# Kernel optimization log

Measured on AMD Instinct MI355X. Metric: run time of the kernel, lower is better.

The kernel has to match this reference:

```python
import jax, jax.numpy as jnp
import numpy as np

N_ELEC = 4096
D_IN = 512
D_MODEL = 512
N_HEADS = 8


def setup_inputs() -> dict:
    key = jax.random.key(0)
    ks = jax.random.split(key, 6)
    scale_in = 1.0 / np.sqrt(D_IN)
    scale_model = 1.0 / np.sqrt(D_MODEL)
    return {
        "hs": jax.random.normal(ks[0], (N_ELEC, D_IN), jnp.float32),
        "hd": jax.random.normal(ks[1], (N_ELEC, D_IN), jnp.float32),
        "qk_kernel": jax.random.normal(ks[2], (D_IN, 2 * D_MODEL), jnp.float32) * scale_in,
        "qk_bias": jnp.zeros((2 * D_MODEL,), jnp.float32),
        "v_kernel": jax.random.normal(ks[3], (D_IN, D_MODEL), jnp.float32) * scale_in,
        "v_bias": jnp.zeros((D_MODEL,), jnp.float32),
        "o_kernel": jax.random.normal(ks[4], (D_MODEL, D_MODEL), jnp.float32) * scale_model,
        "o_bias": jnpp if False else jnp.zeros((D_MODEL,), jnp.float32),
    }


def reference(hs, hd, qk_kernel, qk_bias, v_kernel, v_bias, o_kernel, o_bias):
    n_elec = hs.shape[0]
    # projections
    qk = hs @ qk_kernel + qk_bias          # [N, 2*D]
    q, k = jnp.split(qk, 2, axis=-1)       # each [N, D]
    v = hd @ v_kernel + v_bias             # [N, D]
    # split heads -> [H, N, d_k]
    trans = lambda x: x.reshape(n_elec, N_HEADS, -1).transpose(1, 0, 2)
    q, k, v = trans(q), trans(k), trans(v)
    d_k = q.shape[-1]
    # scaled dot product attention (plain-array fallback path)
    logits = jnp.einsum("hnd,hmd->hnm", q, k) / jnp.sqrt(jnp.asarray(d_k, q.dtype))
    attn = jax.nn.softmax(logits, axis=-1)
    values = jnp.einsum("hnm,hmd->hnd", attn, v)   # [H, N, d_k]
    values = values.transpose(1, 0, 2).reshape(n_elec, D_MODEL)
    out = values @ o_kernel + o_bias
    return out
```

## Files before the change

kernel.cpp:

```cpp
#include <hip/hip_runtime.h>
#include <math.h>

#define N_ELEC 4096
#define DMODEL 512
#define NHEADS 8
#define DK 64

typedef __attribute__((ext_vector_type(8)))  short  bf16x8;
typedef __attribute__((ext_vector_type(4)))  float  f32x4;
typedef __attribute__((ext_vector_type(16))) float  f32x16;
typedef __attribute__((ext_vector_type(8)))  ushort u16x8;
typedef __attribute__((ext_vector_type(4)))  ushort u16x4;

__device__ __forceinline__ int swz(int r, int c) { return r * 64 + (c ^ ((r & 7) * 8)); }

__device__ __forceinline__ ushort f2bf(float f) {
  union { float f; unsigned int u; } cv; cv.f = f;
  unsigned int u = cv.u;
  u += 0x7FFFu + ((u >> 16) & 1u);
  return (ushort)(u >> 16);
}

__device__ __forceinline__ unsigned cvtpk(float lo, float hi) {
  unsigned r;
  asm("v_cvt_pk_bf16_f32 %0, %1, %2" : "=v"(r) : "v"(lo), "v"(hi));
  return r;
}

#define PLSWAP(a, b) asm volatile("v_permlane32_swap_b32 %0, %1" : "+v"(a), "+v"(b))

#define GLL16(gp, lp) __builtin_amdgcn_global_load_lds( \
    (const __attribute__((address_space(1))) void*)(gp), \
    (__attribute__((address_space(3))) void*)(lp), 16, 0, 0)

#define QK_LOG2E 0.18033688f

__global__ __launch_bounds__(256) void prep(
    const float* __restrict__ hs, const float* __restrict__ hd,
    const float* __restrict__ qk_w, const float* __restrict__ v_w, const float* __restrict__ o_w,
    ushort* __restrict__ hsb, ushort* __restrict__ hdb,
    ushort* __restrict__ wqkT, ushort* __restrict__ wvT, ushort* __restrict__ woT)
{
  __shared__ float Ts[64][68];
  const int b = blockIdx.x, t = threadIdx.x;
  if (b < 2048) {
    const float* in = (b < 1024) ? hs : hd;
    ushort* outp = (b < 1024) ? hsb : hdb;
    const int idx = ((b & 1023) * 256 + t) * 8;
    float4 a = *(const float4*)(in + idx);
    float4 b2 = *(const float4*)(in + idx + 4);
    u16x8 o;
    o[0] = f2bf(a.x); o[1] = f2bf(a.y); o[2] = f2bf(a.z); o[3] = f2bf(a.w);
    o[4] = f2bf(b2.x); o[5] = f2bf(b2.y); o[6] = f2bf(b2.z); o[7] = f2bf(b2.w);
    *(u16x8*)(outp + idx) = o;
    return;
  }
  const float* in; ushort* outp; int C, tb;
  if (b < 2176)      { in = qk_w; outp = wqkT; C = 1024; tb = b - 2048; }
  else if (b < 2240) { in = v_w;  outp = wvT;  C = 512;  tb = b - 2176; }
  else               { in = o_w;  outp = woT;  C = 512;  tb = b - 2240; }
  const int ctiles = C >> 6;
  const int ct = (tb % ctiles) * 64, rt = (tb / ctiles) * 64;
  const int lr = t >> 4, lc4 = (t & 15) * 4;
#pragma unroll
  for (int rep = 0; rep < 4; ++rep) {
    const int r = lr + rep * 16;
    float4 v = *(const float4*)(in + (size_t)(rt + r) * C + ct + lc4);
    Ts[r][lc4] = v.x; Ts[r][lc4 + 1] = v.y; Ts[r][lc4 + 2] = v.z; Ts[r][lc4 + 3] = v.w;
  }
  __syncthreads();
#pragma unroll
  for (int rep = 0; rep < 4; ++rep) {
    const int c = lr + rep * 16;
    u16x4 o;
    o[0] = f2bf(Ts[lc4 + 0][c]); o[1] = f2bf(Ts[lc4 + 1][c]);
    o[2] = f2bf(Ts[lc4 + 2][c]); o[3] = f2bf(Ts[lc4 + 3][c]);
    *(u16x4*)(outp + (size_t)(ct + c) * 512 + rt + lc4) = o;
  }
}

template<int MODE>
__device__ __forceinline__ void proj128_body(
    ushort (&At)[2][128 * 64], ushort (&Bt)[2][128 * 64],
    const int mt, const int nt,
    const ushort* __restrict__ Wt, const ushort* __restrict__ Act,
    const float* __restrict__ bias, void* __restrict__ outp)
{
  const int t = threadIdx.x, w = t >> 6, lane = t & 63;
  const int fr = lane & 15, fp = lane >> 4;

  const ushort* rowsA = (MODE == 1) ? Act + (size_t)mt * 128 * 512 : Wt + (size_t)nt * 128 * 512;
  const ushort* rowsB = (MODE == 1) ? Wt + (size_t)nt * 128 * 512 : Act + (size_t)mt * 128 * 512;

#define STAGEP(buf, k0) do { \
  _Pragma("unroll") \
  for (int rep = 0; rep < 4; ++rep) { \
    const int cid = rep * 256 + t; \
    const int row_ = cid >> 3; \
    const int sc = ((cid & 7) ^ (row_ & 7)) * 8; \
    GLL16(rowsA + (size_t)row_ * 512 + (k0) + sc, &At[buf][(rep * 256 + w * 64) * 8]); \
    GLL16(rowsB + (size_t)row_ * 512 + (k0) + sc, &Bt[buf][(rep * 256 + w * 64) * 8]); \
  } \
} while (0)

  const int rbase = (w >> 1) * 64;
  const int cbase = (w & 1) * 64;

  f32x4 acc[16];
#pragma unroll
  for (int i = 0; i < 16; ++i) acc[i] = (f32x4){0.f, 0.f, 0.f, 0.f};

  STAGEP(0, 0);
  asm volatile("s_waitcnt vmcnt(0)" ::: "memory");
  __syncthreads();

  for (int it = 0; it < 8; ++it) {
    const int cur = it & 1;
    if (it < 7) STAGEP(cur ^ 1, (it + 1) * 64);
#pragma unroll
    for (int kh = 0; kh < 2; ++kh) {
      bf16x8 af[4], bf[4];
#pragma unroll
      for (int i = 0; i < 4; ++i) {
        af[i] = *(const bf16x8*)&At[cur][swz(rbase + i * 16 + fr, kh * 32 + fp * 8)];
        bf[i] = *(const bf16x8*)&Bt[cur][swz(cbase + i * 16 + fr, kh * 32 + fp * 8)];
      }
#pragma unroll
      for (int i = 0; i < 4; ++i)
#pragma unroll
        for (int j = 0; j < 4; ++j)
          acc[i * 4 + j] = __builtin_amdgcn_mfma_f32_16x16x32_bf16(af[i], bf[j], acc[i * 4 + j], 0, 0, 0);
    }
    asm volatile("s_waitcnt vmcnt(0)" ::: "memory");
    __syncthreads();
  }
#undef STAGEP

  if (MODE == 0) {
    ushort* out = (ushort*)outp;
#pragma unroll
    for (int i = 0; i < 4; ++i) {
      const int nb = nt * 128 + rbase + i * 16 + fp * 4;
      const float scale = (nb < 512) ? QK_LOG2E : 1.0f;
      const float4 bb = *(const float4*)(bias + nb);
      const int h = nb >> 6, d0 = nb & 63;
#pragma unroll
      for (int j = 0; j < 4; ++j) {
        const int m = mt * 128 + cbase + j * 16 + fr;
        const f32x4 a = acc[i * 4 + j];
        u16x4 o;
        o[0] = f2bf((a[0] + bb.x) * scale); o[1] = f2bf((a[1] + bb.y) * scale);
        o[2] = f2bf((a[2] + bb.z) * scale); o[3] = f2bf((a[3] + bb.w) * scale);
        *(u16x4*)(out + (size_t)h * N_ELEC * DK + (size_t)m * DK + d0) = o;
      }
    }
  } else if (MODE == 1) {
    ushort* out = (ushort*)outp;
#pragma unroll
    for (int j = 0; j < 4; ++j) {
      const int n = nt * 128 + cbase + j * 16 + fr;
      const float bb = bias[n];
      const int h = n >> 6, dd = n & 63;
#pragma unroll
      for (int i = 0; i < 4; ++i) {
        const int m0 = mt * 128 + rbase + i * 16 + fp * 4;
        const f32x4 a = acc[i * 4 + j];
        u16x4 o;
        o[0] = f2bf(a[0] + bb); o[1] = f2bf(a[1] + bb);
        o[2] = f2bf(a[2] + bb); o[3] = f2bf(a[3] + bb);
        *(u16x4*)(out + (size_t)h * DK * N_ELEC + (size_t)dd * N_ELEC + m0) = o;
      }
    }
  } else {
    float* out = (float*)outp;
#pragma unroll
    for (int i = 0; i < 4; ++i) {
      const int n0 = nt * 128 + rbase + i * 16 + fp * 4;
      const float4 bb = *(const float4*)(bias + n0);
#pragma unroll
      for (int j = 0; j < 4; ++j) {
        const int m = mt * 128 + cbase + j * 16 + fr;
        const f32x4 a = acc[i * 4 + j];
        float4 o;
        o.x = a[0] + bb.x; o.y = a[1] + bb.y; o.z = a[2] + bb.z; o.w = a[3] + bb.w;
        *(float4*)(out + (size_t)m * DMODEL + n0) = o;
      }
    }
  }
}

__global__ __launch_bounds__(256) void projQKV(
    const ushort* __restrict__ wqkT, const ushort* __restrict__ hsb,
    const ushort* __restrict__ hdb,  const ushort* __restrict__ wvT,
    const float* __restrict__ qk_b,  const float* __restrict__ v_b,
    ushort* __restrict__ qbuf, ushort* __restrict__ vbufT)
{
  __shared__ ushort At[2][128 * 64];
  __shared__ ushort Bt[2][128 * 64];
  if (blockIdx.y < 8) proj128_body<0>(At, Bt, blockIdx.x, blockIdx.y,     wqkT, hsb, qk_b, qbuf);
  else                proj128_body<1>(At, Bt, blockIdx.x, blockIdx.y - 8, wvT,  hdb, v_b,  vbufT);
}

__global__ __launch_bounds__(256) void projO(
    const ushort* __restrict__ woT, const ushort* __restrict__ Act,
    const float* __restrict__ bias, float* __restrict__ outp)
{
  __shared__ ushort At[2][128 * 64];
  __shared__ ushort Bt[2][128 * 64];
  proj128_body<2>(At, Bt, blockIdx.x, blockIdx.y, woT, Act, bias, outp);
}

template<int SPLIT>
__global__ __launch_bounds__(256, 4) void attn(
    const ushort* __restrict__ qb, const ushort* __restrict__ kb,
    const ushort* __restrict__ vtb, ushort* __restrict__ vals,
    float* __restrict__ Opart, float2* __restrict__ ML)
{
  __shared__ ushort Ks[2][64 * 64], Vts[2][64 * 64];
  const int bid = blockIdx.x;
  const int h = bid & 7, qt = (bid >> 3) & 31, s = bid >> 8;
  const int t = threadIdx.x, w = t >> 6, lane = t & 63;
  const int ql = lane & 31, hi = lane >> 5;
  const int KCH = N_ELEC / SPLIT;

  const ushort* kp = kb  + (size_t)h * N_ELEC * DK + (size_t)s * KCH * DK;
  const ushort* vp = vtb + (size_t)h * DK * N_ELEC + (size_t)s * KCH;
  const int q = qt * 128 + w * 32 + ql;

  bf16x8 qf[4];
  {
    const ushort* qrow = qb + (size_t)h * N_ELEC * DK + (size_t)q * DK + hi * 8;
#pragma unroll
    for (int kc = 0; kc < 4; ++kc) qf[kc] = *(const bf16x8*)(qrow + kc * 16);
  }

  const int srow = lane >> 3;
  const int schunk = ((lane & 7) ^ srow) * 8;

#define STAGE(buf, j0) do { \
  _Pragma("unroll") \
  for (int p = 0; p < 2; ++p) { \
    const int rr = (w * 2 + p) * 8 + srow; \
    GLL16(kp + (size_t)((j0) + rr) * DK + schunk, &Ks[buf][(w * 2 + p) * 512]); \
    GLL16(vp + (size_t)rr * N_ELEC + (j0) + schunk, &Vts[buf][(w * 2 + p) * 512]); \
  } \
} while (0)

  float mrun = -INFINITY, lsum = 0.f;
  f32x16 oa0, oa1;
#pragma unroll
  for (int i = 0; i < 16; ++i) { oa0[i] = 0.f; oa1[i] = 0.f; }

  STAGE(0, 0);
  asm volatile("s_waitcnt vmcnt(0)" ::: "memory");
  __syncthreads();

  for (int it = 0; it < KCH / 64; ++it) {
    const int cur = it & 1;
    if ((it + 1) * 64 < KCH) STAGE(cur ^ 1, (it + 1) * 64);

    f32x16 s0, s1;
#pragma unroll
    for (int i = 0; i < 16; ++i) { s0[i] = 0.f; s1[i] = 0.f; }
    __builtin_amdgcn_s_setprio(1);
#pragma unroll
    for (int kc = 0; kc < 4; ++kc) {
      bf16x8 ka0 = *(const bf16x8*)&Ks[cur][swz(ql,      (kc * 2 + hi) * 8)];
      bf16x8 ka1 = *(const bf16x8*)&Ks[cur][swz(32 + ql, (kc * 2 + hi) * 8)];
      s0 = __builtin_amdgcn_mfma_f32_32x32x16_bf16(ka0, qf[kc], s0, 0, 0, 0);
      s1 = __builtin_amdgcn_mfma_f32_32x32x16_bf16(ka1, qf[kc], s1, 0, 0, 0);
    }
    __builtin_amdgcn_s_setprio(0);

    float pm = -INFINITY;
#pragma unroll
    for (int i = 0; i < 16; ++i) pm = fmaxf(pm, fmaxf(s0[i], s1[i]));
    pm = fmaxf(pm, __shfl_xor(pm, 32));
    if (__any(pm > mrun)) {
      const float mnew = fmaxf(mrun, pm);
      const float corr = __builtin_amdgcn_exp2f(mrun - mnew);
      lsum *= corr;
#pragma unroll
      for (int i = 0; i < 16; ++i) { oa0[i] *= corr; oa1[i] *= corr; }
      mrun = mnew;
    }
    float rs = 0.f;
#pragma unroll
    for (int i = 0; i < 16; ++i) {
      s0[i] = __builtin_amdgcn_exp2f(s0[i] - mrun); rs += s0[i];
      s1[i] = __builtin_amdgcn_exp2f(s1[i] - mrun); rs += s1[i];
    }
    rs += __shfl_xor(rs, 32);
    lsum += rs;

    unsigned pb[4][4];
#pragma unroll
    for (int jc = 0; jc < 4; ++jc) {
      const int base = (jc & 1) * 8;
      unsigned A0, B0, A1, B1;
      if (jc < 2) {
        A0 = cvtpk(s0[base + 0], s0[base + 1]); B0 = cvtpk(s0[base + 4], s0[base + 5]);
        A1 = cvtpk(s0[base + 2], s0[base + 3]); B1 = cvtpk(s0[base + 6], s0[base + 7]);
      } else {
        A0 = cvtpk(s1[base + 0], s1[base + 1]); B0 = cvtpk(s1[base + 4], s1[base + 5]);
        A1 = cvtpk(s1[base + 2], s1[base + 3]); B1 = cvtpk(s1[base + 6], s1[base + 7]);
      }
      PLSWAP(A0, B0);
      PLSWAP(A1, B1);
      pb[jc][0] = A0; pb[jc][1] = A1; pb[jc][2] = B0; pb[jc][3] = B1;
    }

    __builtin_amdgcn_s_setprio(1);
#pragma unroll
    for (int jc = 0; jc < 4; ++jc) {
      union { unsigned u[4]; bf16x8 v; } bu;
      bu.u[0] = pb[jc][0]; bu.u[1] = pb[jc][1]; bu.u[2] = pb[jc][2]; bu.u[3] = pb[jc][3];
      bf16x8 va0 = *(const bf16x8*)&Vts[cur][swz(ql,      (jc * 2 + hi) * 8)];
      bf16x8 va1 = *(const bf16x8*)&Vts[cur][swz(32 + ql, (jc * 2 + hi) * 8)];
      oa0 = __builtin_amdgcn_mfma_f32_32x32x16_bf16(va0, bu.v, oa0, 0, 0, 0);
      oa1 = __builtin_amdgcn_mfma_f32_32x32x16_bf16(va1, bu.v, oa1, 0, 0, 0);
    }
    __builtin_amdgcn_s_setprio(0);

    asm volatile("s_waitcnt vmcnt(0)" ::: "memory");
    __syncthreads();
  }
#undef STAGE

  if constexpr (SPLIT == 1) {
    const float inv = 1.f / lsum;
#pragma unroll
    for (int dt = 0; dt < 2; ++dt) {
      const f32x16& oo = dt ? oa1 : oa0;
#pragma unroll
      for (int a = 0; a < 4; ++a) {
        const int d0 = dt * 32 + a * 8 + hi * 4;
        u16x4 o;
#pragma unroll
        for (int g = 0; g < 4; ++g) o[g] = f2bf(oo[a * 4 + g] * inv);
        *(u16x4*)(vals + (size_t)q * DMODEL + h * DK + d0) = o;
      }
    }
  } else {
    float* ob = Opart + ((size_t)(s * NHEADS + h) * N_ELEC + q) * DK;
#pragma unroll
    for (int dt = 0; dt < 2; ++dt) {
      const f32x16& oo = dt ? oa1 : oa0;
#pragma unroll
      for (int a = 0; a < 4; ++a) {
        float4 o;
        o.x = oo[a * 4 + 0]; o.y = oo[a * 4 + 1]; o.z = oo[a * 4 + 2]; o.w = oo[a * 4 + 3];
        *(float4*)(ob + dt * 32 + a * 8 + hi * 4) = o;
      }
    }
    if (hi == 0) ML[(size_t)(s * NHEADS + h) * N_ELEC + q] = make_float2(mrun, lsum);
  }
}

template<int NS>
__global__ __launch_bounds__(256) void combine(
    const float* __restrict__ Opart, const float2* __restrict__ ML,
    ushort* __restrict__ vals)
{
  const int rid = blockIdx.x * 4 + (threadIdx.x >> 6);
  const int d = threadIdx.x & 63;
  const int hh = rid >> 12, qq = rid & 4095;
  const size_t base = (size_t)rid * DK + d;
  const size_t sstride = (size_t)NHEADS * N_ELEC * DK;
  float2 mls[NS];
  float m = -INFINITY;
#pragma unroll
  for (int i = 0; i < NS; ++i) {
    mls[i] = ML[(size_t)i * NHEADS * N_ELEC + rid];
    m = fmaxf(m, mls[i].x);
  }
  float l = 0.f, o = 0.f;
#pragma unroll
  for (int i = 0; i < NS; ++i) {
    const float c = __builtin_amdgcn_exp2f(mls[i].x - m);
    l += c * mls[i].y;
    o += c * Opart[i * sstride + base];
  }
  vals[(size_t)qq * DMODEL + hh * DK + d] = f2bf(o / l);
}

extern "C" void kernel_launch(void* const* d_in, const int* in_sizes, int n_in,
                              void* d_out, int out_size, void* d_ws, size_t ws_size,
                              hipStream_t stream) {
  const float* hs   = (const float*)d_in[0];
  const float* hd   = (const float*)d_in[1];
  const float* qk_w = (const float*)d_in[2];
  const float* qk_b = (const float*)d_in[3];
  const float* v_w  = (const float*)d_in[4];
  const float* v_b  = (const float*)d_in[5];
  const float* o_w  = (const float*)d_in[6];
  const float* o_b  = (const float*)d_in[7];
  float* out = (float*)d_out;

  ushort* ws    = (ushort*)d_ws;
  ushort* hsb   = ws;
  ushort* hdb   = hsb  + (size_t)N_ELEC * DMODEL;
  ushort* wqkT  = hdb  + (size_t)N_ELEC * DMODEL;
  ushort* wvT   = wqkT + (size_t)1024 * 512;
  ushort* woT   = wvT  + (size_t)512 * 512;
  ushort* qbuf  = woT  + (size_t)512 * 512;
  ushort* kbuf  = qbuf + (size_t)NHEADS * N_ELEC * DK;
  ushort* vbufT = kbuf + (size_t)NHEADS * N_ELEC * DK;
  ushort* valsb = vbufT + (size_t)NHEADS * DK * N_ELEC;
  float*  Opart = (float*)(valsb + (size_t)N_ELEC * DMODEL);
  float2* ML4   = (float2*)(Opart + (size_t)4 * NHEADS * N_ELEC * DK);
  float2* ML2   = (float2*)(Opart + (size_t)2 * NHEADS * N_ELEC * DK);
  const size_t need4 = (size_t)((char*)(ML4 + (size_t)4 * NHEADS * N_ELEC) - (char*)d_ws);
  const size_t need2 = (size_t)((char*)(ML2 + (size_t)2 * NHEADS * N_ELEC) - (char*)d_ws);

  dim3 blk(256);
  prep<<<dim3(2304), blk, 0, stream>>>(hs, hd, qk_w, v_w, o_w, hsb, hdb, wqkT, wvT, woT);
  projQKV<<<dim3(32, 12), blk, 0, stream>>>(wqkT, hsb, hdb, wvT, qk_b, v_b, qbuf, vbufT);

  if (ws_size >= need4) {
    attn<4><<<dim3(1024), blk, 0, stream>>>(qbuf, kbuf, vbufT, nullptr, Opart, ML4);
    combine<4><<<dim3(NHEADS * N_ELEC / 4), blk, 0, stream>>>(Opart, ML4, valsb);
  } else if (ws_size >= need2) {
    attn<2><<<dim3(512), blk, 0, stream>>>(qbuf, kbuf, vbufT, nullptr, Opart, ML2);
    combine<2><<<dim3(NHEADS * N_ELEC / 4), blk, 0, stream>>>(Opart, ML2, valsb);
  } else {
    attn<1><<<dim3(256), blk, 0, stream>>>(qbuf, kbuf, vbufT, valsb, nullptr, nullptr);
  }

  projO<<<dim3(32, 4), blk, 0, stream>>>(woT, valsb, o_b, out);
}
```

Baseline: 102.3 us.

## Process two query groups per wave in attention to reuse K/V tiles

Each wave now handles 64 query rows (two 32-row groups) instead of 32. Every K and V fragment read from LDS feeds twice as many MFMAs, and each staged K/V tile serves 256 queries per block. The grid is halved and launch bounds drop to 2 blocks per CU to make room for the doubled accumulator registers. The cost is lower occupancy and fewer blocks (512 on the split-4 path) to fill 256 CUs, which leaves less latency hiding across waves.

```diff
diff --git a/kernel.cpp b/kernel.cpp
--- a/kernel.cpp
+++ b/kernel.cpp
@@ -211,27 +211,28 @@
 }
 
 template<int SPLIT>
-__global__ __launch_bounds__(256, 4) void attn(
+__global__ __launch_bounds__(256, 2) void attn(
     const ushort* __restrict__ qb, const ushort* __restrict__ kb,
     const ushort* __restrict__ vtb, ushort* __restrict__ vals,
     float* __restrict__ Opart, float2* __restrict__ ML)
 {
   __shared__ ushort Ks[2][64 * 64], Vts[2][64 * 64];
   const int bid = blockIdx.x;
-  const int h = bid & 7, qt = (bid >> 3) & 31, s = bid >> 8;
+  const int h = bid & 7, qt = (bid >> 3) & 15, s = bid >> 7;
   const int t = threadIdx.x, w = t >> 6, lane = t & 63;
   const int ql = lane & 31, hi = lane >> 5;
   const int KCH = N_ELEC / SPLIT;
 
   const ushort* kp = kb  + (size_t)h * N_ELEC * DK + (size_t)s * KCH * DK;
   const ushort* vp = vtb + (size_t)h * DK * N_ELEC + (size_t)s * KCH;
-  const int q = qt * 128 + w * 32 + ql;
-
-  bf16x8 qf[4];
-  {
-    const ushort* qrow = qb + (size_t)h * N_ELEC * DK + (size_t)q * DK + hi * 8;
-#pragma unroll
-    for (int kc = 0; kc < 4; ++kc) qf[kc] = *(const bf16x8*)(qrow + kc * 16);
+  const int q0 = qt * 256 + w * 64;
+
+  bf16x8 qf[2][4];
+#pragma unroll
+  for (int qg = 0; qg < 2; ++qg) {
+    const ushort* qrow = qb + (size_t)h * N_ELEC * DK + (size_t)(q0 + qg * 32 + ql) * DK + hi * 8;
+#pragma unroll
+    for (int kc = 0; kc < 4; ++kc) qf[qg][kc] = *(const bf16x8*)(qrow + kc * 16);
   }
 
   const int srow = lane >> 3;
@@ -246,10 +247,12 @@
   } \
 } while (0)
 
-  float mrun = -INFINITY, lsum = 0.f;
-  f32x16 oa0, oa1;
-#pragma unroll
-  for (int i = 0; i < 16; ++i) { oa0[i] = 0.f; oa1[i] = 0.f; }
+  float mrun[2] = {-INFINITY, -INFINITY}, lsum[2] = {0.f, 0.f};
+  f32x16 oa0[2], oa1[2];
+#pragma unroll
+  for (int qg = 0; qg < 2; ++qg)
+#pragma unroll
+    for (int i = 0; i < 16; ++i) { oa0[qg][i] = 0.f; oa1[qg][i] = 0.f; }
 
   STAGE(0, 0);
   asm volatile("s_waitcnt vmcnt(0)" ::: "memory");
@@ -259,66 +262,78 @@
     const int cur = it & 1;
     if ((it + 1) * 64 < KCH) STAGE(cur ^ 1, (it + 1) * 64);
 
-    f32x16 s0, s1;
-#pragma unroll
-    for (int i = 0; i < 16; ++i) { s0[i] = 0.f; s1[i] = 0.f; }
+    f32x16 s0[2], s1[2];
+#pragma unroll
+    for (int qg = 0; qg < 2; ++qg)
+#pragma unroll
+      for (int i = 0; i < 16; ++i) { s0[qg][i] = 0.f; s1[qg][i] = 0.f; }
     __builtin_amdgcn_s_setprio(1);
 #pragma unroll
     for (int kc = 0; kc < 4; ++kc) {
       bf16x8 ka0 = *(const bf16x8*)&Ks[cur][swz(ql,      (kc * 2 + hi) * 8)];
       bf16x8 ka1 = *(const bf16x8*)&Ks[cur][swz(32 + ql, (kc * 2 + hi) * 8)];
-      s0 = __builtin_amdgcn_mfma_f32_32x32x16_bf16(ka0, qf[kc], s0, 0, 0, 0);
-      s1 = __builtin_amdgcn_mfma_f32_32x32x16_bf16(ka1, qf[kc], s1, 0, 0, 0);
+#pragma unroll
+      for (int qg = 0; qg < 2; ++qg) {
+        s0[qg] = __builtin_amdgcn_mfma_f32_32x32x16_bf16(ka0, qf[qg][kc], s0[qg], 0, 0, 0);
+        s1[qg] = __builtin_amdgcn_mfma_f32_32x32x16_bf16(ka1, qf[qg][kc], s1[qg], 0, 0, 0);
+      }
     }
     __builtin_amdgcn_s_setprio(0);
 
-    float pm = -INFINITY;
-#pragma unroll
-    for (int i = 0; i < 16; ++i) pm = fmaxf(pm, fmaxf(s0[i], s1[i]));
-    pm = fmaxf(pm, __shfl_xor(pm, 32));
-    if (__any(pm > mrun)) {
-      const float mnew = fmaxf(mrun, pm);
-      const float corr = __builtin_amdgcn_exp2f(mrun - mnew);
-      lsum *= corr;
-#pragma unroll
-      for (int i = 0; i < 16; ++i) { oa0[i] *= corr; oa1[i] *= corr; }
-      mrun = mnew;
-    }
-    float rs = 0.f;
-#pragma unroll
-    for (int i = 0; i < 16; ++i) {
-      s0[i] = __builtin_amdgcn_exp2f(s0[i] - mrun); rs += s0[i];
-      s1[i] = __builtin_amdgcn_exp2f(s1[i] - mrun); rs += s1[i];
-    }
-    rs += __shfl_xor(rs, 32);
-    lsum += rs;
-
-    unsigned pb[4][4];
+    unsigned pb[2][4][4];
+#pragma unroll
+    for (int qg = 0; qg < 2; ++qg) {
+      float pm = -INFINITY;
+#pragma unroll
+      for (int i = 0; i < 16; ++i) pm = fmaxf(pm, fmaxf(s0[qg][i], s1[qg][i]));
+      pm = fmaxf(pm, __shfl_xor(pm, 32));
+      if (__any(pm > mrun[qg])) {
+        const float mnew = fmaxf(mrun[qg], pm);
+        const float corr = __builtin_amdgcn_exp2f(mrun[qg] - mnew);
+        lsum[qg] *= corr;
+#pragma unroll
+        for (int i = 0; i < 16; ++i) { oa0[qg][i] *= corr; oa1[qg][i] *= corr; }
+        mrun[qg] = mnew;
+      }
+      float rs = 0.f;
+#pragma unroll
+      for (int i = 0; i < 16; ++i) {
+        s0[qg][i] = __builtin_amdgcn_exp2f(s0[qg][i] - mrun[qg]); rs += s0[qg][i];
+        s1[qg][i] = __builtin_amdgcn_exp2f(s1[qg][i] - mrun[qg]); rs += s1[qg][i];
+      }
+      rs += __shfl_xor(rs, 32);
+      lsum[qg] += rs;
+
+#pragma unroll
+      for (int jc = 0; jc < 4; ++jc) {
+        const int base = (jc & 1) * 8;
+        unsigned A0, B0, A1, B1;
+        if (jc < 2) {
+          A0 = cvtpk(s0[qg][base + 0], s0[qg][base + 1]); B0 = cvtpk(s0[qg][base + 4], s0[qg][base + 5]);
+          A1 = cvtpk(s0[qg][base + 2], s0[qg][base + 3]); B1 = cvtpk(s0[qg][base + 6], s0[qg][base + 7]);
+        } else {
+          A0 = cvtpk(s1[qg][base + 0], s1[qg][base + 1]); B0 = cvtpk(s1[qg][base + 4], s1[qg][base + 5]);
+          A1 = cvtpk(s1[qg][base + 2], s1[qg][base + 3]); B1 = cvtpk(s1[qg][base + 6], s1[qg][base + 7]);
+        }
+        PLSWAP(A0, B0);
+        PLSWAP(A1, B1);
+        pb[qg][jc][0] = A0; pb[qg][jc][1] = A1; pb[qg][jc][2] = B0; pb[qg][jc][3] = B1;
+      }
+    }
+
+    __builtin_amdgcn_s_setprio(1);
 #pragma unroll
     for (int jc = 0; jc < 4; ++jc) {
-      const int base = (jc & 1) * 8;
-      unsigned A0, B0, A1, B1;
-      if (jc < 2) {
-        A0 = cvtpk(s0[base + 0], s0[base + 1]); B0 = cvtpk(s0[base + 4], s0[base + 5]);
-        A1 = cvtpk(s0[base + 2], s0[base + 3]); B1 = cvtpk(s0[base + 6], s0[base + 7]);
-      } else {
-        A0 = cvtpk(s1[base + 0], s1[base + 1]); B0 = cvtpk(s1[base + 4], s1[base + 5]);
-        A1 = cvtpk(s1[base + 2], s1[base + 3]); B1 = cvtpk(s1[base + 6], s1[base + 7]);
-      }
-      PLSWAP(A0, B0);
-      PLSWAP(A1, B1);
-      pb[jc][0] = A0; pb[jc][1] = A1; pb[jc][2] = B0; pb[jc][3] = B1;
-    }
-
-    __builtin_amdgcn_s_setprio(1);
-#pragma unroll
-    for (int jc = 0; jc < 4; ++jc) {
-      union { unsigned u[4]; bf16x8 v; } bu;
-      bu.u[0] = pb[jc][0]; bu.u[1] = pb[jc][1]; bu.u[2] = pb[jc][2]; bu.u[3] = pb[jc][3];
       bf16x8 va0 = *(const bf16x8*)&Vts[cur][swz(ql,      (jc * 2 + hi) * 8)];
       bf16x8 va1 = *(const bf16x8*)&Vts[cur][swz(32 + ql, (jc * 2 + hi) * 8)];
-      oa0 = __builtin_amdgcn_mfma_f32_32x32x16_bf16(va0, bu.v, oa0, 0, 0, 0);
-      oa1 = __builtin_amdgcn_mfma_f32_32x32x16_bf16(va1, bu.v, oa1, 0, 0, 0);
+#pragma unroll
+      for (int qg = 0; qg < 2; ++qg) {
+        union { unsigned u[4]; bf16x8 v; } bu;
+        bu.u[0] = pb[qg][jc][0]; bu.u[1] = pb[qg][jc][1];
+        bu.u[2] = pb[qg][jc][2]; bu.u[3] = pb[qg][jc][3];
+        oa0[qg] = __builtin_amdgcn_mfma_f32_32x32x16_bf16(va0, bu.v, oa0[qg], 0, 0, 0);
+        oa1[qg] = __builtin_amdgcn_mfma_f32_32x32x16_bf16(va1, bu.v, oa1[qg], 0, 0, 0);
+      }
     }
     __builtin_amdgcn_s_setprio(0);
 
@@ -327,33 +342,37 @@
   }
 #undef STAGE
 
-  if constexpr (SPLIT == 1) {
-    const float inv = 1.f / lsum;
-#pragma unroll
-    for (int dt = 0; dt < 2; ++dt) {
-      const f32x16& oo = dt ? oa1 : oa0;
-#pragma unroll
-      for (int a = 0; a < 4; ++a) {
-        const int d0 = dt * 32 + a * 8 + hi * 4;
-        u16x4 o;
-#pragma unroll
-        for (int g = 0; g < 4; ++g) o[g] = f2bf(oo[a * 4 + g] * inv);
-        *(u16x4*)(vals + (size_t)q * DMODEL + h * DK + d0) = o;
-      }
-    }
-  } else {
-    float* ob = Opart + ((size_t)(s * NHEADS + h) * N_ELEC + q) * DK;
-#pragma unroll
-    for (int dt = 0; dt < 2; ++dt) {
-      const f32x16& oo = dt ? oa1 : oa0;
-#pragma unroll
-      for (int a = 0; a < 4; ++a) {
-        float4 o;
-        o.x = oo[a * 4 + 0]; o.y = oo[a * 4 + 1]; o.z = oo[a * 4 + 2]; o.w = oo[a * 4 + 3];
-        *(float4*)(ob + dt * 32 + a * 8 + hi * 4) = o;
-      }
-    }
-    if (hi == 0) ML[(size_t)(s * NHEADS + h) * N_ELEC + q] = make_float2(mrun, lsum);
+#pragma unroll
+  for (int qg = 0; qg < 2; ++qg) {
+    const int q = q0 + qg * 32 + ql;
+    if constexpr (SPLIT == 1) {
+      const float inv = 1.f / lsum[qg];
+#pragma unroll
+      for (int dt = 0; dt < 2; ++dt) {
+        const f32x16& oo = dt ? oa1[qg] : oa0[qg];
+#pragma unroll
+        for (int a = 0; a < 4; ++a) {
+          const int d0 = dt * 32 + a * 8 + hi * 4;
+          u16x4 o;
+#pragma unroll
+          for (int g = 0; g < 4; ++g) o[g] = f2bf(oo[a * 4 + g] * inv);
+          *(u16x4*)(vals + (size_t)q * DMODEL + h * DK + d0) = o;
+        }
+      }
+    } else {
+      float* ob = Opart + ((size_t)(s * NHEADS + h) * N_ELEC + q) * DK;
+#pragma unroll
+      for (int dt = 0; dt < 2; ++dt) {
+        const f32x16& oo = dt ? oa1[qg] : oa0[qg];
+#pragma unroll
+        for (int a = 0; a < 4; ++a) {
+          float4 o;
+          o.x = oo[a * 4 + 0]; o.y = oo[a * 4 + 1]; o.z = oo[a * 4 + 2]; o.w = oo[a * 4 + 3];
+          *(float4*)(ob + dt * 32 + a * 8 + hi * 4) = o;
+        }
+      }
+      if (hi == 0) ML[(size_t)(s * NHEADS + h) * N_ELEC + q] = make_float2(mrun[qg], lsum[qg]);
+    }
   }
 }
 
@@ -418,13 +437,13 @@
   projQKV<<<dim3(32, 12), blk, 0, stream>>>(wqkT, hsb, hdb, wvT, qk_b, v_b, qbuf, vbufT);
 
   if (ws_size >= need4) {
-    attn<4><<<dim3(1024), blk, 0, stream>>>(qbuf, kbuf, vbufT, nullptr, Opart, ML4);
+    attn<4><<<dim3(512), blk, 0, stream>>>(qbuf, kbuf, vbufT, nullptr, Opart, ML4);
     combine<4><<<dim3(NHEADS * N_ELEC / 4), blk, 0, stream>>>(Opart, ML4, valsb);
   } else if (ws_size >= need2) {
-    attn<2><<<dim3(512), blk, 0, stream>>>(qbuf, kbuf, vbufT, nullptr, Opart, ML2);
+    attn<2><<<dim3(256), blk, 0, stream>>>(qbuf, kbuf, vbufT, nullptr, Opart, ML2);
     combine<2><<<dim3(NHEADS * N_ELEC / 4), blk, 0, stream>>>(Opart, ML2, valsb);
   } else {
-    attn<1><<<dim3(256), blk, 0, stream>>>(qbuf, kbuf, vbufT, valsb, nullptr, nullptr);
+    attn<1><<<dim3(128), blk, 0, stream>>>(qbuf, kbuf, vbufT, valsb, nullptr, nullptr);
   }
 
   projO<<<dim3(32, 4), blk, 0, stream>>>(woT, valsb, o_b, out);
```

Result: no change. 100.8 us (-1.5%).
